# Optimization experiments

Measured on AMD Instinct MI355X. Metric: run time of the kernel, lower is better.

## Reference

```python
import jax, jax.numpy as jnp
import numpy as np

# Gemma-style paged attention, decode-heavy continuous batching
B = 16            # number of sequences in the batch
BLOCK = 64        # KV-cache block size (tokens per block)
MAX_BLOCKS = 32   # max blocks per sequence -> max 2048 KV tokens
NUM_BLOCKS = B * MAX_BLOCKS  # 512 total cache blocks
MAX_KV = MAX_BLOCKS * BLOCK  # 2048
HQ, HK, D = 16, 8, 256       # query heads, kv heads (GQA), head_dim
HIDDEN = 3072
MAX_Q = 4                    # max new (query) tokens per sequence
ROPE_BASE = 10000.0


def setup_inputs() -> dict:
    key = jax.random.key(0)
    ks = jax.random.split(key, 7)
    # deterministic ragged layout
    q_seqlens = np.array([1 + (i % 4) for i in range(B)], np.int64)        # sum = 40
    kv_seqlens = np.array([1024 + (i * 67) % 1025 for i in range(B)], np.int64)
    q_start_loc = np.concatenate([[0], np.cumsum(q_seqlens)[:-1]]).astype(np.int64)
    T = int(q_seqlens.sum())
    history = kv_seqlens - q_seqlens
    position_ids_1d = np.concatenate(
        [np.arange(history[i], kv_seqlens[i]) for i in range(B)]).astype(np.int64)
    block_offsets = np.arange(NUM_BLOCKS, dtype=np.int64).reshape(B, MAX_BLOCKS)
    inv_freq = (1.0 / ROPE_BASE ** (np.arange(0, D, 2) / D)).astype(np.float32)
    return {
        'hidden_states': jax.random.normal(ks[0], (T, HIDDEN), jnp.float32),
        'Wq': jax.random.normal(ks[1], (HIDDEN, HQ * D), jnp.float32) * 0.02,
        'Wk': jax.random.normal(ks[2], (HIDDEN, HK * D), jnp.float32) * 0.02,
        'Wv': jax.random.normal(ks[3], (HIDDEN, HK * D), jnp.float32) * 0.02,
        'Wo': jax.random.normal(ks[4], (HQ * D, HIDDEN), jnp.float32) * 0.02,
        'k_cache': jax.random.normal(ks[5], (NUM_BLOCKS, BLOCK, HK, D), jnp.float32),
        'v_cache': jax.random.normal(ks[6], (NUM_BLOCKS, BLOCK, HK, D), jnp.float32),
        'inv_freq': jnp.asarray(inv_freq),
        'position_ids_1d': jnp.asarray(position_ids_1d),
        'q_start_loc': jnp.asarray(q_start_loc),
        'q_seqlens': jnp.asarray(q_seqlens),
        'kv_seqlens': jnp.asarray(kv_seqlens),
        'block_offsets': jnp.asarray(block_offsets),
    }


def reference(hidden_states, Wq, Wk, Wv, Wo, k_cache, v_cache, inv_freq,
              position_ids_1d, q_start_loc, q_seqlens, kv_seqlens, block_offsets):
    T = hidden_states.shape[0]
    # fused QKV projection
    q = (hidden_states @ Wq).reshape(T, HQ, D)
    k = (hidden_states @ Wk).reshape(T, HK, D)
    v = (hidden_states @ Wv).reshape(T, HK, D)
    # fused rotary embedding (neox / rotate-half style, per-token position ids)
    freqs = position_ids_1d.astype(jnp.float32)[:, None] * inv_freq[None, :]  # [T, D/2]
    cos = jnp.cos(freqs)[:, None, :]
    sin = jnp.sin(freqs)[:, None, :]

    def rope(x):
        x1, x2 = jnp.split(x, 2, axis=-1)
        return jnp.concatenate([x1 * cos - x2 * sin, x2 * cos + x1 * sin], axis=-1)

    q = rope(q)
    k = rope(k)
    # ---- fill_kv_cache: scatter new K/V into paged block cache ----
    tok = jnp.arange(T)
    seq_end = jnp.cumsum(q_seqlens)
    seq_id = jnp.searchsorted(seq_end, tok, side='right')      # sequence of each token
    off = tok - q_start_loc[seq_id]                             # offset within new tokens
    kv_pos = (kv_seqlens - q_seqlens)[seq_id] + off             # absolute kv position
    blk = block_offsets[seq_id, kv_pos // BLOCK]
    slot = kv_pos % BLOCK
    k_cache = k_cache.at[blk, slot].set(k)
    v_cache = v_cache.at[blk, slot].set(v)
    # ---- paged_attention_fwd ----
    # gather each sequence's blocks -> [B, MAX_KV, HK, D]
    k_seq = k_cache[block_offsets].reshape(B, MAX_KV, HK, D)
    v_seq = v_cache[block_offsets].reshape(B, MAX_KV, HK, D)
    # pad queries per sequence -> [B, MAX_Q, HK, G, D]
    qidx = jnp.clip(q_start_loc[:, None] + jnp.arange(MAX_Q)[None, :], 0, T - 1)
    G = HQ // HK
    qpad = q[qidx].reshape(B, MAX_Q, HK, G, D)
    scale = jnp.float32(D) ** -0.5
    scores = jnp.einsum('bqkgd,bskd->bkgqs', qpad * scale, k_seq)  # [B,HK,G,MAX_Q,MAX_KV]
    # causal mask over absolute kv positions (also masks padded kv slots)
    jpos = jnp.arange(MAX_Q)[None, :, None]
    spos = jnp.arange(MAX_KV)[None, None, :]
    mask = spos <= ((kv_seqlens - q_seqlens)[:, None, None] + jpos)  # [B,MAX_Q,MAX_KV]
    scores = jnp.where(mask[:, None, None, :, :], scores, jnp.float32(-1e30))
    attn = jax.nn.softmax(scores, axis=-1)
    out = jnp.einsum('bkgqs,bskd->bqkgd', attn, v_seq).reshape(B, MAX_Q, HQ * D)
    # scatter padded output back to flat token layout
    out_flat = out[seq_id, off]  # [T, HQ*D]
    return out_flat @ Wo
```

## Files before the change

kernel.cpp:

```cpp
#include <hip/hip_runtime.h>
#include <math.h>

#define TT 40
#define NB 16
#define HQn 16
#define HKn 8
#define Gn 2
#define Dn 256
#define HID 3072
#define QKV_COLS 8192
#define NCHUNK 16
#define CHUNKT 128

__global__ __launch_bounds__(256) void k1_qkv_gemm(
    const float* __restrict__ hs, const float* __restrict__ Wq,
    const float* __restrict__ Wk, const float* __restrict__ Wv,
    float* __restrict__ part1) {
  const int tile = blockIdx.x & 31;
  const int ks = blockIdx.x >> 5;
  const int c0 = tile << 8;
  const float* W; int ld, cw0;
  if (tile < 16)      { W = Wq; ld = 4096; cw0 = c0; }
  else if (tile < 24) { W = Wk; ld = 2048; cw0 = c0 - 4096; }
  else                { W = Wv; ld = 2048; cw0 = c0 - 6144; }
  const int kbase = ks * 192;
  const int cq = (threadIdx.x & 63) << 2;
  const int r0 = (threadIdx.x >> 6) * 10;
  __shared__ float h_lds[40][64];
  float acc[10][4];
#pragma unroll
  for (int r = 0; r < 10; ++r) { acc[r][0]=0.f; acc[r][1]=0.f; acc[r][2]=0.f; acc[r][3]=0.f; }
  for (int kc = 0; kc < 192; kc += 64) {
    __syncthreads();
    for (int i = threadIdx.x; i < 2560; i += 256) {
      int t = i >> 6, kk = i & 63;
      h_lds[t][kk] = hs[t * HID + kbase + kc + kk];
    }
    __syncthreads();
    const float* wp = W + (size_t)(kbase + kc) * ld + cw0 + cq;
#pragma unroll 8
    for (int kk = 0; kk < 64; ++kk) {
      float4 w4 = *reinterpret_cast<const float4*>(wp + (size_t)kk * ld);
#pragma unroll
      for (int r = 0; r < 10; ++r) {
        float h = h_lds[r0 + r][kk];
        acc[r][0] = fmaf(h, w4.x, acc[r][0]);
        acc[r][1] = fmaf(h, w4.y, acc[r][1]);
        acc[r][2] = fmaf(h, w4.z, acc[r][2]);
        acc[r][3] = fmaf(h, w4.w, acc[r][3]);
      }
    }
  }
#pragma unroll
  for (int r = 0; r < 10; ++r) {
    int t = r0 + r;
    float4 v = make_float4(acc[r][0], acc[r][1], acc[r][2], acc[r][3]);
    *reinterpret_cast<float4*>(&part1[(size_t)(ks * TT + t) * QKV_COLS + c0 + cq]) = v;
  }
}

__global__ __launch_bounds__(256) void k2_reduce_rope(
    const float* __restrict__ part1, const float* __restrict__ inv_freq,
    const int* __restrict__ pos_ids,
    float* __restrict__ qbuf, float* __restrict__ kbuf, float* __restrict__ vbuf) {
  const int t = blockIdx.x >> 5;
  const int tile = blockIdx.x & 31;
  const int c = (tile << 8) + threadIdx.x;
  float s = 0.f;
#pragma unroll
  for (int ks = 0; ks < 16; ++ks) s += part1[(size_t)(ks * TT + t) * QKV_COLS + c];
  __shared__ float sl[256];
  sl[threadIdx.x] = s;
  __syncthreads();
  if (tile < 24) {
    const int d = threadIdx.x;
    const int d2 = d & 127;
    float fr = (float)pos_ids[t] * inv_freq[d2];
    float cs = cosf(fr), sn = sinf(fr);
    float v = (d < 128) ? (sl[d] * cs - sl[d + 128] * sn)
                        : (sl[d] * cs + sl[d - 128] * sn);
    if (tile < 16) qbuf[t * 4096 + (tile << 8) + d] = v * 0.0625f;
    else           kbuf[t * 2048 + ((tile - 16) << 8) + d] = v;
  } else {
    vbuf[t * 2048 + ((tile - 24) << 8) + threadIdx.x] = s;
  }
}

__global__ __launch_bounds__(256) void k3_attn_partial(
    const float* __restrict__ qbuf, const float* __restrict__ kbuf,
    const float* __restrict__ vbuf, const float* __restrict__ k_cache,
    const float* __restrict__ v_cache, const int* __restrict__ blk_off,
    const int* __restrict__ q_start, const int* __restrict__ q_lens,
    const int* __restrict__ kv_lens,
    float* __restrict__ part_o, float* __restrict__ part_ml) {
  const int chunk = blockIdx.x & 15;
  const int hk = (blockIdx.x >> 4) & 7;
  const int b = blockIdx.x >> 7;
  const int kv_len = kv_lens[b];
  const int cs0 = chunk * CHUNKT;
  if (cs0 >= kv_len) return;
  const int q_cnt = q_lens[b];
  const int hist = kv_len - q_cnt;
  const int q0 = q_start[b];
  const int nq = q_cnt * 2;

  __shared__ float q_lds[8][256];
  __shared__ float S2[2][128][8];
  __shared__ float red[32][8];
  __shared__ float Mg[8];
  __shared__ float obuf[4][8][256];

  const int tid = threadIdx.x;
  const int w = tid >> 6;
  const int lane = tid & 63;
  const int tp = lane & 7;
  const int qd = lane >> 3;

  const int bi = (b << 5) + (cs0 >> 6);
  const int blk0v = blk_off[bi];
  const int blk1v = blk_off[bi + 1];
  const float* kb0  = k_cache + ((size_t)blk0v << 17) + ((size_t)hk << 8);
  const float* kb1  = k_cache + ((size_t)blk1v << 17) + ((size_t)hk << 8);
  const float* vb0  = v_cache + ((size_t)blk0v << 17) + ((size_t)hk << 8);
  const float* vb1  = v_cache + ((size_t)blk1v << 17) + ((size_t)hk << 8);
  const float* knew = kbuf + ((size_t)q0 << 11) + ((size_t)hk << 8);
  const float* vnew = vbuf + ((size_t)q0 << 11) + ((size_t)hk << 8);

  auto rowK = [&](int s) -> const float* {
    if (s < hist) {
      const float* base = (s & 64) ? kb1 : kb0;
      return base + ((size_t)(s & 63) << 11);
    }
    return knew + ((size_t)(s - hist) << 11);
  };
  auto rowV = [&](int s) -> const float* {
    if (s < hist) {
      const float* base = (s & 64) ? vb1 : vb0;
      return base + ((size_t)(s & 63) << 11);
    }
    return vnew + ((size_t)(s - hist) << 11);
  };

  for (int i = tid; i < 2048; i += 256) {
    int qv = i >> 8, d = i & 255;
    int qtok = min(qv >> 1, q_cnt - 1);
    q_lds[qv][d] = qbuf[(size_t)(q0 + qtok) * 4096 + (hk * Gn + (qv & 1)) * 256 + d];
  }
  __syncthreads();

  const int sBeg = cs0 + (w << 5);

  const float* kr[4];
#pragma unroll
  for (int tt = 0; tt < 4; ++tt) {
    int s = sBeg + (tp << 2) + tt;
    int sc = s < kv_len ? s : kv_len - 1;
    kr[tt] = rowK(sc) + (qd << 2);
  }
  float acc[4][8];
#pragma unroll
  for (int tt = 0; tt < 4; ++tt)
#pragma unroll
    for (int qv = 0; qv < 8; ++qv) acc[tt][qv] = 0.f;

#pragma unroll
  for (int c = 0; c < 8; ++c) {
    float4 kf[4];
#pragma unroll
    for (int tt = 0; tt < 4; ++tt)
      kf[tt] = *reinterpret_cast<const float4*>(kr[tt] + (c << 5));
#pragma unroll
    for (int qv = 0; qv < 8; ++qv) {
      float4 qf = *reinterpret_cast<const float4*>(&q_lds[qv][(qd << 2) + (c << 5)]);
#pragma unroll
      for (int tt = 0; tt < 4; ++tt) {
        acc[tt][qv] = fmaf(qf.x, kf[tt].x, acc[tt][qv]);
        acc[tt][qv] = fmaf(qf.y, kf[tt].y, acc[tt][qv]);
        acc[tt][qv] = fmaf(qf.z, kf[tt].z, acc[tt][qv]);
        acc[tt][qv] = fmaf(qf.w, kf[tt].w, acc[tt][qv]);
      }
    }
  }
#pragma unroll
  for (int tt = 0; tt < 4; ++tt)
#pragma unroll
    for (int qv = 0; qv < 8; ++qv) {
      float v = acc[tt][qv];
      v += __shfl_xor(v, 8);
      v += __shfl_xor(v, 16);
      acc[tt][qv] = v;
    }
  if ((lane & 24) == 0) {
    const int h = lane >> 5;
#pragma unroll
    for (int tt = 0; tt < 4; ++tt) {
      int srel = (w << 5) + (tp << 2) + tt;
      *reinterpret_cast<float4*>(&S2[h][srel][0]) =
          make_float4(acc[tt][0], acc[tt][1], acc[tt][2], acc[tt][3]);
      *reinterpret_cast<float4*>(&S2[h][srel][4]) =
          make_float4(acc[tt][4], acc[tt][5], acc[tt][6], acc[tt][7]);
    }
  }
  __syncthreads();

  const int qv2 = tid & 7;
  const int grp = tid >> 3;
  float sv[4];
  {
    float mloc = -1e30f;
#pragma unroll
    for (int t = 0; t < 4; ++t) {
      int sl = (grp << 2) + t;
      float v = S2[0][sl][qv2] + S2[1][sl][qv2];
      bool valid = (qv2 < nq) && ((cs0 + sl - hist) <= (qv2 >> 1));
      v = valid ? v : -1e30f;
      sv[t] = v;
      mloc = fmaxf(mloc, v);
    }
    red[grp][qv2] = mloc;
  }
  __syncthreads();
  if (tid < 8) {
    float M = -1e30f;
#pragma unroll
    for (int i = 0; i < 32; ++i) M = fmaxf(M, red[i][tid]);
    Mg[tid] = M;
  }
  __syncthreads();
  {
    float M = Mg[qv2];
    float lloc = 0.f;
#pragma unroll
    for (int t = 0; t < 4; ++t) {
      float p = __expf(sv[t] - M);
      S2[0][(grp << 2) + t][qv2] = p;
      lloc += p;
    }
    red[grp][qv2] = lloc;
  }
  __syncthreads();
  if (tid < 8) {
    float L = 0.f;
#pragma unroll
    for (int i = 0; i < 32; ++i) L += red[i][tid];
    int pidx = (((b * HKn + hk) * NCHUNK + chunk) << 3) + tid;
    part_ml[pidx * 2] = Mg[tid];
    part_ml[pidx * 2 + 1] = L;
  }

  float4 pacc[8];
#pragma unroll
  for (int q = 0; q < 8; ++q) pacc[q] = make_float4(0.f, 0.f, 0.f, 0.f);
  const int d4 = lane << 2;
#pragma unroll 4
  for (int t = 0; t < 32; ++t) {
    int s = sBeg + t;
    int sc = s < kv_len ? s : kv_len - 1;
    float4 vf = *reinterpret_cast<const float4*>(rowV(sc) + d4);
    int srel = (w << 5) + t;
    float4 p0 = *reinterpret_cast<const float4*>(&S2[0][srel][0]);
    float4 p1 = *reinterpret_cast<const float4*>(&S2[0][srel][4]);
    float pr[8] = {p0.x, p0.y, p0.z, p0.w, p1.x, p1.y, p1.z, p1.w};
#pragma unroll
    for (int q = 0; q < 8; ++q) {
      pacc[q].x = fmaf(pr[q], vf.x, pacc[q].x);
      pacc[q].y = fmaf(pr[q], vf.y, pacc[q].y);
      pacc[q].z = fmaf(pr[q], vf.z, pacc[q].z);
      pacc[q].w = fmaf(pr[q], vf.w, pacc[q].w);
    }
  }
#pragma unroll
  for (int q = 0; q < 8; ++q)
    *reinterpret_cast<float4*>(&obuf[w][q][d4]) = pacc[q];
  __syncthreads();

  for (int q = 0; q < nq; ++q) {
    float o = obuf[0][q][tid] + obuf[1][q][tid] + obuf[2][q][tid] + obuf[3][q][tid];
    int pidx = (((b * HKn + hk) * NCHUNK + chunk) << 3) + q;
    part_o[(size_t)pidx * 256 + tid] = o;
  }
}

__global__ __launch_bounds__(64) void k4_attn_reduce(
    const float* __restrict__ part_o, const float* __restrict__ part_ml,
    const int* __restrict__ q_start, const int* __restrict__ q_lens,
    const int* __restrict__ kv_lens, float* __restrict__ attn_out) {
  const int h = blockIdx.x & 15;
  const int qtok = (blockIdx.x >> 4) & 3;
  const int b = blockIdx.x >> 6;
  const int q_cnt = q_lens[b];
  if (qtok >= q_cnt) return;
  const int kv_len = kv_lens[b];
  const int nparts = (kv_len + CHUNKT - 1) >> 7;
  const int qv = qtok * 2 + (h & 1);
  const int hk = h >> 1;
  const int lane = threadIdx.x;
  const int pbase = ((b * HKn + hk) * NCHUNK) << 3;
  float2 mls[16];
#pragma unroll
  for (int i = 0; i < 16; ++i)
    if (i < nparts)
      mls[i] = *reinterpret_cast<const float2*>(&part_ml[(size_t)(pbase + (i << 3) + qv) * 2]);
  float M = -1e30f;
#pragma unroll
  for (int i = 0; i < 16; ++i)
    if (i < nparts) M = fmaxf(M, mls[i].x);
  float4 o = make_float4(0.f, 0.f, 0.f, 0.f);
  float L = 0.f;
#pragma unroll
  for (int i = 0; i < 16; ++i)
    if (i < nparts) {
      float corr = __expf(mls[i].x - M);
      L += corr * mls[i].y;
      float4 pv = *reinterpret_cast<const float4*>(
          &part_o[(size_t)(pbase + (i << 3) + qv) * 256 + (lane << 2)]);
      o.x = fmaf(corr, pv.x, o.x);
      o.y = fmaf(corr, pv.y, o.y);
      o.z = fmaf(corr, pv.z, o.z);
      o.w = fmaf(corr, pv.w, o.w);
    }
  float inv = 1.0f / L;
  int tr = q_start[b] + qtok;
  float4 res = make_float4(o.x * inv, o.y * inv, o.z * inv, o.w * inv);
  *reinterpret_cast<float4*>(&attn_out[((size_t)tr * HQn + h) * 256 + (lane << 2)]) = res;
}

__global__ __launch_bounds__(256) void k5_out_gemm(
    const float* __restrict__ ain, const float* __restrict__ Wo,
    float* __restrict__ part2) {
  const int tile = blockIdx.x % 12;
  const int ks = blockIdx.x / 12;
  const int c0 = tile << 8;
  const int kbase = ks << 7;
  const int cq = (threadIdx.x & 63) << 2;
  const int r0 = (threadIdx.x >> 6) * 10;
  __shared__ float h_lds[40][64];
  float acc[10][4];
#pragma unroll
  for (int r = 0; r < 10; ++r) { acc[r][0]=0.f; acc[r][1]=0.f; acc[r][2]=0.f; acc[r][3]=0.f; }
  for (int kc = 0; kc < 128; kc += 64) {
    __syncthreads();
    for (int i = threadIdx.x; i < 2560; i += 256) {
      int t = i >> 6, kk = i & 63;
      h_lds[t][kk] = ain[(size_t)t * 4096 + kbase + kc + kk];
    }
    __syncthreads();
    const float* wp = Wo + (size_t)(kbase + kc) * 3072 + c0 + cq;
#pragma unroll 8
    for (int kk = 0; kk < 64; ++kk) {
      float4 w4 = *reinterpret_cast<const float4*>(wp + (size_t)kk * 3072);
#pragma unroll
      for (int r = 0; r < 10; ++r) {
        float h = h_lds[r0 + r][kk];
        acc[r][0] = fmaf(h, w4.x, acc[r][0]);
        acc[r][1] = fmaf(h, w4.y, acc[r][1]);
        acc[r][2] = fmaf(h, w4.z, acc[r][2]);
        acc[r][3] = fmaf(h, w4.w, acc[r][3]);
      }
    }
  }
#pragma unroll
  for (int r = 0; r < 10; ++r) {
    int t = r0 + r;
    float4 v = make_float4(acc[r][0], acc[r][1], acc[r][2], acc[r][3]);
    *reinterpret_cast<float4*>(&part2[(size_t)(ks * TT + t) * 3072 + c0 + cq]) = v;
  }
}

__global__ __launch_bounds__(256) void k6_final_reduce(
    const float* __restrict__ part2, float* __restrict__ out) {
  const int idx = blockIdx.x * 256 + threadIdx.x;
  float s = 0.f;
#pragma unroll
  for (int ks = 0; ks < 32; ++ks) s += part2[(size_t)ks * 122880 + idx];
  out[idx] = s;
}

extern "C" void kernel_launch(void* const* d_in, const int* in_sizes, int n_in,
                              void* d_out, int out_size, void* d_ws, size_t ws_size,
                              hipStream_t stream) {
  const float* hs       = (const float*)d_in[0];
  const float* Wq       = (const float*)d_in[1];
  const float* Wk       = (const float*)d_in[2];
  const float* Wv       = (const float*)d_in[3];
  const float* Wo       = (const float*)d_in[4];
  const float* k_cache  = (const float*)d_in[5];
  const float* v_cache  = (const float*)d_in[6];
  const float* inv_freq = (const float*)d_in[7];
  const int*   pos_ids  = (const int*)d_in[8];
  const int*   q_start  = (const int*)d_in[9];
  const int*   q_lens   = (const int*)d_in[10];
  const int*   kv_lens  = (const int*)d_in[11];
  const int*   blk_off  = (const int*)d_in[12];

  float* ws = (float*)d_ws;
  float* qbuf     = ws;
  float* kbuf     = ws + 163840;
  float* vbuf     = ws + 245760;
  float* attn_out = ws + 327680;
  float* big      = ws + 491520;
  float* part1    = big;
  float* part_o   = big;
  float* part_ml  = big + 4194304;
  float* part2    = big;
  float* out      = (float*)d_out;

  k1_qkv_gemm<<<512, 256, 0, stream>>>(hs, Wq, Wk, Wv, part1);
  k2_reduce_rope<<<1280, 256, 0, stream>>>(part1, inv_freq, pos_ids, qbuf, kbuf, vbuf);
  k3_attn_partial<<<2048, 256, 0, stream>>>(qbuf, kbuf, vbuf, k_cache, v_cache,
                                            blk_off, q_start, q_lens, kv_lens,
                                            part_o, part_ml);
  k4_attn_reduce<<<1024, 64, 0, stream>>>(part_o, part_ml, q_start, q_lens,
                                          kv_lens, attn_out);
  k5_out_gemm<<<384, 256, 0, stream>>>(attn_out, Wo, part2);
  k6_final_reduce<<<480, 256, 0, stream>>>(part2, out);
}
```

Baseline: 290.6 us.

## Fuse all six kernels into one persistent cooperative kernel with grid syncs

Replaces the six separate launches (QKV GEMM, reduce+RoPE, attention partial, attention reduce, output GEMM, final reduce) with a single cooperative persistent kernel. Each stage loops over its original work items with a grid-stride loop, and stages are separated by grid-wide syncs. Shared memory is carved from one buffer. The aim is to remove per-launch overhead and inter-kernel gaps. In exchange, occupancy is capped at 3 blocks per CU with a grid of at most 768, each stage carries grid-sync cost, and the 50KB shared allocation may limit residency.

Result: slower. 679.3 us (+133.8%).

```diff
diff --git a/kernel.cpp b/kernel.cpp
--- a/kernel.cpp
+++ b/kernel.cpp
@@ -1,5 +1,8 @@
 #include <hip/hip_runtime.h>
+#include <hip/hip_cooperative_groups.h>
 #include <math.h>
+
+namespace cg = cooperative_groups;
 
 #define TT 40
 #define NB 16
@@ -11,369 +14,390 @@
 #define QKV_COLS 8192
 #define NCHUNK 16
 #define CHUNKT 128
-
-__global__ __launch_bounds__(256) void k1_qkv_gemm(
+#define MAXGRID 768
+
+__global__ __launch_bounds__(256, 3) void mega(
     const float* __restrict__ hs, const float* __restrict__ Wq,
     const float* __restrict__ Wk, const float* __restrict__ Wv,
-    float* __restrict__ part1) {
-  const int tile = blockIdx.x & 31;
-  const int ks = blockIdx.x >> 5;
-  const int c0 = tile << 8;
-  const float* W; int ld, cw0;
-  if (tile < 16)      { W = Wq; ld = 4096; cw0 = c0; }
-  else if (tile < 24) { W = Wk; ld = 2048; cw0 = c0 - 4096; }
-  else                { W = Wv; ld = 2048; cw0 = c0 - 6144; }
-  const int kbase = ks * 192;
-  const int cq = (threadIdx.x & 63) << 2;
-  const int r0 = (threadIdx.x >> 6) * 10;
-  __shared__ float h_lds[40][64];
-  float acc[10][4];
-#pragma unroll
-  for (int r = 0; r < 10; ++r) { acc[r][0]=0.f; acc[r][1]=0.f; acc[r][2]=0.f; acc[r][3]=0.f; }
-  for (int kc = 0; kc < 192; kc += 64) {
-    __syncthreads();
-    for (int i = threadIdx.x; i < 2560; i += 256) {
-      int t = i >> 6, kk = i & 63;
-      h_lds[t][kk] = hs[t * HID + kbase + kc + kk];
+    const float* __restrict__ Wo, const float* __restrict__ k_cache,
+    const float* __restrict__ v_cache, const float* __restrict__ inv_freq,
+    const int* __restrict__ pos_ids, const int* __restrict__ q_start,
+    const int* __restrict__ q_lens, const int* __restrict__ kv_lens,
+    const int* __restrict__ blk_off,
+    float* __restrict__ qbuf, float* __restrict__ kbuf, float* __restrict__ vbuf,
+    float* __restrict__ attn_out, float* __restrict__ part1,
+    float* __restrict__ part_o, float* __restrict__ part_ml,
+    float* __restrict__ part2, float* __restrict__ out) {
+  cg::grid_group grd = cg::this_grid();
+  __shared__ __align__(16) char smem[50240];
+  const int tid = threadIdx.x;
+  const int NGRID = gridDim.x;
+
+  {
+    float (*h_lds)[64] = (float (*)[64])smem;
+    for (int v = blockIdx.x; v < 512; v += NGRID) {
+      const int tile = v & 31;
+      const int ks = v >> 5;
+      const int c0 = tile << 8;
+      const float* W; int ld, cw0;
+      if (tile < 16)      { W = Wq; ld = 4096; cw0 = c0; }
+      else if (tile < 24) { W = Wk; ld = 2048; cw0 = c0 - 4096; }
+      else                { W = Wv; ld = 2048; cw0 = c0 - 6144; }
+      const int kbase = ks * 192;
+      const int cq = (tid & 63) << 2;
+      const int r0 = (tid >> 6) * 10;
+      float acc[10][4];
+#pragma unroll
+      for (int r = 0; r < 10; ++r) { acc[r][0]=0.f; acc[r][1]=0.f; acc[r][2]=0.f; acc[r][3]=0.f; }
+      for (int kc = 0; kc < 192; kc += 64) {
+        __syncthreads();
+        for (int i = tid; i < 2560; i += 256) {
+          int t = i >> 6, kk = i & 63;
+          h_lds[t][kk] = hs[t * HID + kbase + kc + kk];
+        }
+        __syncthreads();
+        const float* wp = W + (size_t)(kbase + kc) * ld + cw0 + cq;
+#pragma unroll 8
+        for (int kk = 0; kk < 64; ++kk) {
+          float4 w4 = *reinterpret_cast<const float4*>(wp + (size_t)kk * ld);
+#pragma unroll
+          for (int r = 0; r < 10; ++r) {
+            float h = h_lds[r0 + r][kk];
+            acc[r][0] = fmaf(h, w4.x, acc[r][0]);
+            acc[r][1] = fmaf(h, w4.y, acc[r][1]);
+            acc[r][2] = fmaf(h, w4.z, acc[r][2]);
+            acc[r][3] = fmaf(h, w4.w, acc[r][3]);
+          }
+        }
+      }
+#pragma unroll
+      for (int r = 0; r < 10; ++r) {
+        int t = r0 + r;
+        float4 vv = make_float4(acc[r][0], acc[r][1], acc[r][2], acc[r][3]);
+        *reinterpret_cast<float4*>(&part1[(size_t)(ks * TT + t) * QKV_COLS + c0 + cq]) = vv;
+      }
+      __syncthreads();
     }
-    __syncthreads();
-    const float* wp = W + (size_t)(kbase + kc) * ld + cw0 + cq;
+  }
+  grd.sync();
+
+  {
+    float* sl = (float*)smem;
+    for (int v = blockIdx.x; v < 1280; v += NGRID) {
+      const int t = v >> 5;
+      const int tile = v & 31;
+      const int c = (tile << 8) + tid;
+      float s = 0.f;
+#pragma unroll
+      for (int ks = 0; ks < 16; ++ks) s += part1[(size_t)(ks * TT + t) * QKV_COLS + c];
+      __syncthreads();
+      sl[tid] = s;
+      __syncthreads();
+      if (tile < 24) {
+        const int d = tid;
+        const int d2 = d & 127;
+        float fr = (float)pos_ids[t] * inv_freq[d2];
+        float cs = cosf(fr), sn = sinf(fr);
+        float val = (d < 128) ? (sl[d] * cs - sl[d + 128] * sn)
+                              : (sl[d] * cs + sl[d - 128] * sn);
+        if (tile < 16) qbuf[t * 4096 + (tile << 8) + d] = val * 0.0625f;
+        else           kbuf[t * 2048 + ((tile - 16) << 8) + d] = val;
+      } else {
+        vbuf[t * 2048 + ((tile - 24) << 8) + tid] = s;
+      }
+      __syncthreads();
+    }
+  }
+  grd.sync();
+
+  {
+    float (*q_lds)[256] = (float (*)[256])smem;
+    float (*S2)[8]      = (float (*)[8])(smem + 8192);
+    float (*red)[8]     = (float (*)[8])(smem + 16384);
+    float* Mg           = (float*)(smem + 17408);
+    float (*obuf)[256]  = (float (*)[256])(smem + 17472);
+    const int w = tid >> 6;
+    const int lane = tid & 63;
+    const int tp = lane & 7;
+    const int qd = lane >> 3;
+
+    for (int v = blockIdx.x; v < 2048; v += NGRID) {
+      const int chunk = v & 15;
+      const int hk = (v >> 4) & 7;
+      const int b = v >> 7;
+      const int kv_len = kv_lens[b];
+      const int cs0 = chunk * CHUNKT;
+      if (cs0 < kv_len) {
+        const int q_cnt = q_lens[b];
+        const int hist = kv_len - q_cnt;
+        const int q0 = q_start[b];
+        const int nq = q_cnt * 2;
+
+        const int bi = (b << 5) + (cs0 >> 6);
+        const int blk0v = blk_off[bi];
+        const int blk1v = blk_off[bi + 1];
+        const float* kb0  = k_cache + ((size_t)blk0v << 17) + ((size_t)hk << 8);
+        const float* kb1  = k_cache + ((size_t)blk1v << 17) + ((size_t)hk << 8);
+        const float* vb0  = v_cache + ((size_t)blk0v << 17) + ((size_t)hk << 8);
+        const float* vb1  = v_cache + ((size_t)blk1v << 17) + ((size_t)hk << 8);
+        const float* knew = kbuf + ((size_t)q0 << 11) + ((size_t)hk << 8);
+        const float* vnew = vbuf + ((size_t)q0 << 11) + ((size_t)hk << 8);
+
+        auto rowK = [&](int s) -> const float* {
+          if (s < hist) {
+            const float* base = (s & 64) ? kb1 : kb0;
+            return base + ((size_t)(s & 63) << 11);
+          }
+          return knew + ((size_t)(s - hist) << 11);
+        };
+        auto rowV = [&](int s) -> const float* {
+          if (s < hist) {
+            const float* base = (s & 64) ? vb1 : vb0;
+            return base + ((size_t)(s & 63) << 11);
+          }
+          return vnew + ((size_t)(s - hist) << 11);
+        };
+
+        __syncthreads();
+        for (int i = tid; i < 2048; i += 256) {
+          int qv = i >> 8, d = i & 255;
+          int qtok = min(qv >> 1, q_cnt - 1);
+          q_lds[qv][d] = qbuf[(size_t)(q0 + qtok) * 4096 + (hk * Gn + (qv & 1)) * 256 + d];
+        }
+        __syncthreads();
+
+        const int sBeg = cs0 + (w << 5);
+
+        const float* kr[4];
+#pragma unroll
+        for (int tt = 0; tt < 4; ++tt) {
+          int s = sBeg + (tp << 2) + tt;
+          int sc = s < kv_len ? s : kv_len - 1;
+          kr[tt] = rowK(sc) + (qd << 2);
+        }
+        float acc[4][8];
+#pragma unroll
+        for (int tt = 0; tt < 4; ++tt)
+#pragma unroll
+          for (int qv = 0; qv < 8; ++qv) acc[tt][qv] = 0.f;
+#pragma unroll
+        for (int c = 0; c < 8; ++c) {
+          float4 kf[4];
+#pragma unroll
+          for (int tt = 0; tt < 4; ++tt)
+            kf[tt] = *reinterpret_cast<const float4*>(kr[tt] + (c << 5));
+#pragma unroll
+          for (int qv = 0; qv < 8; ++qv) {
+            float4 qf = *reinterpret_cast<const float4*>(&q_lds[qv][(qd << 2) + (c << 5)]);
+#pragma unroll
+            for (int tt = 0; tt < 4; ++tt) {
+              acc[tt][qv] = fmaf(qf.x, kf[tt].x, acc[tt][qv]);
+              acc[tt][qv] = fmaf(qf.y, kf[tt].y, acc[tt][qv]);
+              acc[tt][qv] = fmaf(qf.z, kf[tt].z, acc[tt][qv]);
+              acc[tt][qv] = fmaf(qf.w, kf[tt].w, acc[tt][qv]);
+            }
+          }
+        }
+#pragma unroll
+        for (int tt = 0; tt < 4; ++tt)
+#pragma unroll
+          for (int qv = 0; qv < 8; ++qv) {
+            float val = acc[tt][qv];
+            val += __shfl_xor(val, 8);
+            val += __shfl_xor(val, 16);
+            acc[tt][qv] = val;
+          }
+        if ((lane & 24) == 0) {
+          const int h = lane >> 5;
+#pragma unroll
+          for (int tt = 0; tt < 4; ++tt) {
+            int srel = (w << 5) + (tp << 2) + tt;
+            *reinterpret_cast<float4*>(&S2[(h << 7) + srel][0]) =
+                make_float4(acc[tt][0], acc[tt][1], acc[tt][2], acc[tt][3]);
+            *reinterpret_cast<float4*>(&S2[(h << 7) + srel][4]) =
+                make_float4(acc[tt][4], acc[tt][5], acc[tt][6], acc[tt][7]);
+          }
+        }
+        __syncthreads();
+
+        const int qv2 = tid & 7;
+        const int grp = tid >> 3;
+        float sv[4];
+        {
+          float mloc = -1e30f;
+#pragma unroll
+          for (int t = 0; t < 4; ++t) {
+            int sl2 = (grp << 2) + t;
+            float val = S2[sl2][qv2] + S2[128 + sl2][qv2];
+            bool valid = (qv2 < nq) && ((cs0 + sl2 - hist) <= (qv2 >> 1));
+            val = valid ? val : -1e30f;
+            sv[t] = val;
+            mloc = fmaxf(mloc, val);
+          }
+          red[grp][qv2] = mloc;
+        }
+        __syncthreads();
+        if (tid < 8) {
+          float M = -1e30f;
+#pragma unroll
+          for (int i = 0; i < 32; ++i) M = fmaxf(M, red[i][tid]);
+          Mg[tid] = M;
+        }
+        __syncthreads();
+        {
+          float M = Mg[qv2];
+          float lloc = 0.f;
+#pragma unroll
+          for (int t = 0; t < 4; ++t) {
+            float p = __expf(sv[t] - M);
+            S2[(grp << 2) + t][qv2] = p;
+            lloc += p;
+          }
+          red[grp][qv2] = lloc;
+        }
+        __syncthreads();
+        if (tid < 8) {
+          float L = 0.f;
+#pragma unroll
+          for (int i = 0; i < 32; ++i) L += red[i][tid];
+          int pidx = (((b * HKn + hk) * NCHUNK + chunk) << 3) + tid;
+          part_ml[pidx * 2] = Mg[tid];
+          part_ml[pidx * 2 + 1] = L;
+        }
+
+        float4 pacc[8];
+#pragma unroll
+        for (int q = 0; q < 8; ++q) pacc[q] = make_float4(0.f, 0.f, 0.f, 0.f);
+        const int d4 = lane << 2;
+#pragma unroll 4
+        for (int t = 0; t < 32; ++t) {
+          int s = sBeg + t;
+          int sc = s < kv_len ? s : kv_len - 1;
+          float4 vf = *reinterpret_cast<const float4*>(rowV(sc) + d4);
+          int srel = (w << 5) + t;
+          float4 p0 = *reinterpret_cast<const float4*>(&S2[srel][0]);
+          float4 p1 = *reinterpret_cast<const float4*>(&S2[srel][4]);
+          float pr[8] = {p0.x, p0.y, p0.z, p0.w, p1.x, p1.y, p1.z, p1.w};
+#pragma unroll
+          for (int q = 0; q < 8; ++q) {
+            pacc[q].x = fmaf(pr[q], vf.x, pacc[q].x);
+            pacc[q].y = fmaf(pr[q], vf.y, pacc[q].y);
+            pacc[q].z = fmaf(pr[q], vf.z, pacc[q].z);
+            pacc[q].w = fmaf(pr[q], vf.w, pacc[q].w);
+          }
+        }
+#pragma unroll
+        for (int q = 0; q < 8; ++q)
+          *reinterpret_cast<float4*>(&obuf[w * 8 + q][d4]) = pacc[q];
+        __syncthreads();
+
+        for (int q = 0; q < nq; ++q) {
+          float o = obuf[q][tid] + obuf[8 + q][tid] + obuf[16 + q][tid] + obuf[24 + q][tid];
+          int pidx = (((b * HKn + hk) * NCHUNK + chunk) << 3) + q;
+          part_o[(size_t)pidx * 256 + tid] = o;
+        }
+        __syncthreads();
+      }
+    }
+  }
+  grd.sync();
+
+  {
+    const int w = tid >> 6;
+    const int lane = tid & 63;
+    for (int u = blockIdx.x * 4 + w; u < 1024; u += NGRID * 4) {
+      const int h = u & 15;
+      const int qtok = (u >> 4) & 3;
+      const int b = u >> 6;
+      const int q_cnt = q_lens[b];
+      if (qtok < q_cnt) {
+        const int kv_len = kv_lens[b];
+        const int nparts = (kv_len + CHUNKT - 1) >> 7;
+        const int qv = qtok * 2 + (h & 1);
+        const int hk = h >> 1;
+        const int pbase = ((b * HKn + hk) * NCHUNK) << 3;
+        float2 mls[16];
+#pragma unroll
+        for (int i = 0; i < 16; ++i)
+          if (i < nparts)
+            mls[i] = *reinterpret_cast<const float2*>(&part_ml[(size_t)(pbase + (i << 3) + qv) * 2]);
+        float M = -1e30f;
+#pragma unroll
+        for (int i = 0; i < 16; ++i)
+          if (i < nparts) M = fmaxf(M, mls[i].x);
+        float4 o = make_float4(0.f, 0.f, 0.f, 0.f);
+        float L = 0.f;
+#pragma unroll
+        for (int i = 0; i < 16; ++i)
+          if (i < nparts) {
+            float corr = __expf(mls[i].x - M);
+            L += corr * mls[i].y;
+            float4 pv = *reinterpret_cast<const float4*>(
+                &part_o[(size_t)(pbase + (i << 3) + qv) * 256 + (lane << 2)]);
+            o.x = fmaf(corr, pv.x, o.x);
+            o.y = fmaf(corr, pv.y, o.y);
+            o.z = fmaf(corr, pv.z, o.z);
+            o.w = fmaf(corr, pv.w, o.w);
+          }
+        float inv = 1.0f / L;
+        int tr = q_start[b] + qtok;
+        float4 res = make_float4(o.x * inv, o.y * inv, o.z * inv, o.w * inv);
+        *reinterpret_cast<float4*>(&attn_out[((size_t)tr * HQn + h) * 256 + (lane << 2)]) = res;
+      }
+    }
+  }
+  grd.sync();
+
+  {
+    float (*h_lds)[64] = (float (*)[64])smem;
+    for (int v = blockIdx.x; v < 384; v += NGRID) {
+      const int tile = v % 12;
+      const int ks = v / 12;
+      const int c0 = tile << 8;
+      const int kbase = ks << 7;
+      const int cq = (tid & 63) << 2;
+      const int r0 = (tid >> 6) * 10;
+      float acc[10][4];
+#pragma unroll
+      for (int r = 0; r < 10; ++r) { acc[r][0]=0.f; acc[r][1]=0.f; acc[r][2]=0.f; acc[r][3]=0.f; }
+      for (int kc = 0; kc < 128; kc += 64) {
+        __syncthreads();
+        for (int i = tid; i < 2560; i += 256) {
+          int t = i >> 6, kk = i & 63;
+          h_lds[t][kk] = attn_out[(size_t)t * 4096 + kbase + kc + kk];
+        }
+        __syncthreads();
+        const float* wp = Wo + (size_t)(kbase + kc) * 3072 + c0 + cq;
 #pragma unroll 8
-    for (int kk = 0; kk < 64; ++kk) {
-      float4 w4 = *reinterpret_cast<const float4*>(wp + (size_t)kk * ld);
+        for (int kk = 0; kk < 64; ++kk) {
+          float4 w4 = *reinterpret_cast<const float4*>(wp + (size_t)kk * 3072);
+#pragma unroll
+          for (int r = 0; r < 10; ++r) {
+            float h = h_lds[r0 + r][kk];
+            acc[r][0] = fmaf(h, w4.x, acc[r][0]);
+            acc[r][1] = fmaf(h, w4.y, acc[r][1]);
+            acc[r][2] = fmaf(h, w4.z, acc[r][2]);
+            acc[r][3] = fmaf(h, w4.w, acc[r][3]);
+          }
+        }
+      }
 #pragma unroll
       for (int r = 0; r < 10; ++r) {
-        float h = h_lds[r0 + r][kk];
-        acc[r][0] = fmaf(h, w4.x, acc[r][0]);
-        acc[r][1] = fmaf(h, w4.y, acc[r][1]);
-        acc[r][2] = fmaf(h, w4.z, acc[r][2]);
-        acc[r][3] = fmaf(h, w4.w, acc[r][3]);
-      }
+        int t = r0 + r;
+        float4 vv = make_float4(acc[r][0], acc[r][1], acc[r][2], acc[r][3]);
+        *reinterpret_cast<float4*>(&part2[(size_t)(ks * TT + t) * 3072 + c0 + cq]) = vv;
+      }
+      __syncthreads();
     }
   }
-#pragma unroll
-  for (int r = 0; r < 10; ++r) {
-    int t = r0 + r;
-    float4 v = make_float4(acc[r][0], acc[r][1], acc[r][2], acc[r][3]);
-    *reinterpret_cast<float4*>(&part1[(size_t)(ks * TT + t) * QKV_COLS + c0 + cq]) = v;
-  }
-}
-
-__global__ __launch_bounds__(256) void k2_reduce_rope(
-    const float* __restrict__ part1, const float* __restrict__ inv_freq,
-    const int* __restrict__ pos_ids,
-    float* __restrict__ qbuf, float* __restrict__ kbuf, float* __restrict__ vbuf) {
-  const int t = blockIdx.x >> 5;
-  const int tile = blockIdx.x & 31;
-  const int c = (tile << 8) + threadIdx.x;
-  float s = 0.f;
-#pragma unroll
-  for (int ks = 0; ks < 16; ++ks) s += part1[(size_t)(ks * TT + t) * QKV_COLS + c];
-  __shared__ float sl[256];
-  sl[threadIdx.x] = s;
-  __syncthreads();
-  if (tile < 24) {
-    const int d = threadIdx.x;
-    const int d2 = d & 127;
-    float fr = (float)pos_ids[t] * inv_freq[d2];
-    float cs = cosf(fr), sn = sinf(fr);
-    float v = (d < 128) ? (sl[d] * cs - sl[d + 128] * sn)
-                        : (sl[d] * cs + sl[d - 128] * sn);
-    if (tile < 16) qbuf[t * 4096 + (tile << 8) + d] = v * 0.0625f;
-    else           kbuf[t * 2048 + ((tile - 16) << 8) + d] = v;
-  } else {
-    vbuf[t * 2048 + ((tile - 24) << 8) + threadIdx.x] = s;
-  }
-}
-
-__global__ __launch_bounds__(256) void k3_attn_partial(
-    const float* __restrict__ qbuf, const float* __restrict__ kbuf,
-    const float* __restrict__ vbuf, const float* __restrict__ k_cache,
-    const float* __restrict__ v_cache, const int* __restrict__ blk_off,
-    const int* __restrict__ q_start, const int* __restrict__ q_lens,
-    const int* __restrict__ kv_lens,
-    float* __restrict__ part_o, float* __restrict__ part_ml) {
-  const int chunk = blockIdx.x & 15;
-  const int hk = (blockIdx.x >> 4) & 7;
-  const int b = blockIdx.x >> 7;
-  const int kv_len = kv_lens[b];
-  const int cs0 = chunk * CHUNKT;
-  if (cs0 >= kv_len) return;
-  const int q_cnt = q_lens[b];
-  const int hist = kv_len - q_cnt;
-  const int q0 = q_start[b];
-  const int nq = q_cnt * 2;
-
-  __shared__ float q_lds[8][256];
-  __shared__ float S2[2][128][8];
-  __shared__ float red[32][8];
-  __shared__ float Mg[8];
-  __shared__ float obuf[4][8][256];
-
-  const int tid = threadIdx.x;
-  const int w = tid >> 6;
-  const int lane = tid & 63;
-  const int tp = lane & 7;
-  const int qd = lane >> 3;
-
-  const int bi = (b << 5) + (cs0 >> 6);
-  const int blk0v = blk_off[bi];
-  const int blk1v = blk_off[bi + 1];
-  const float* kb0  = k_cache + ((size_t)blk0v << 17) + ((size_t)hk << 8);
-  const float* kb1  = k_cache + ((size_t)blk1v << 17) + ((size_t)hk << 8);
-  const float* vb0  = v_cache + ((size_t)blk0v << 17) + ((size_t)hk << 8);
-  const float* vb1  = v_cache + ((size_t)blk1v << 17) + ((size_t)hk << 8);
-  const float* knew = kbuf + ((size_t)q0 << 11) + ((size_t)hk << 8);
-  const float* vnew = vbuf + ((size_t)q0 << 11) + ((size_t)hk << 8);
-
-  auto rowK = [&](int s) -> const float* {
-    if (s < hist) {
-      const float* base = (s & 64) ? kb1 : kb0;
-      return base + ((size_t)(s & 63) << 11);
-    }
-    return knew + ((size_t)(s - hist) << 11);
-  };
-  auto rowV = [&](int s) -> const float* {
-    if (s < hist) {
-      const float* base = (s & 64) ? vb1 : vb0;
-      return base + ((size_t)(s & 63) << 11);
-    }
-    return vnew + ((size_t)(s - hist) << 11);
-  };
-
-  for (int i = tid; i < 2048; i += 256) {
-    int qv = i >> 8, d = i & 255;
-    int qtok = min(qv >> 1, q_cnt - 1);
-    q_lds[qv][d] = qbuf[(size_t)(q0 + qtok) * 4096 + (hk * Gn + (qv & 1)) * 256 + d];
-  }
-  __syncthreads();
-
-  const int sBeg = cs0 + (w << 5);
-
-  const float* kr[4];
-#pragma unroll
-  for (int tt = 0; tt < 4; ++tt) {
-    int s = sBeg + (tp << 2) + tt;
-    int sc = s < kv_len ? s : kv_len - 1;
-    kr[tt] = rowK(sc) + (qd << 2);
-  }
-  float acc[4][8];
-#pragma unroll
-  for (int tt = 0; tt < 4; ++tt)
-#pragma unroll
-    for (int qv = 0; qv < 8; ++qv) acc[tt][qv] = 0.f;
-
-#pragma unroll
-  for (int c = 0; c < 8; ++c) {
-    float4 kf[4];
-#pragma unroll
-    for (int tt = 0; tt < 4; ++tt)
-      kf[tt] = *reinterpret_cast<const float4*>(kr[tt] + (c << 5));
-#pragma unroll
-    for (int qv = 0; qv < 8; ++qv) {
-      float4 qf = *reinterpret_cast<const float4*>(&q_lds[qv][(qd << 2) + (c << 5)]);
-#pragma unroll
-      for (int tt = 0; tt < 4; ++tt) {
-        acc[tt][qv] = fmaf(qf.x, kf[tt].x, acc[tt][qv]);
-        acc[tt][qv] = fmaf(qf.y, kf[tt].y, acc[tt][qv]);
-        acc[tt][qv] = fmaf(qf.z, kf[tt].z, acc[tt][qv]);
-        acc[tt][qv] = fmaf(qf.w, kf[tt].w, acc[tt][qv]);
-      }
-    }
-  }
-#pragma unroll
-  for (int tt = 0; tt < 4; ++tt)
-#pragma unroll
-    for (int qv = 0; qv < 8; ++qv) {
-      float v = acc[tt][qv];
-      v += __shfl_xor(v, 8);
-      v += __shfl_xor(v, 16);
-      acc[tt][qv] = v;
-    }
-  if ((lane & 24) == 0) {
-    const int h = lane >> 5;
-#pragma unroll
-    for (int tt = 0; tt < 4; ++tt) {
-      int srel = (w << 5) + (tp << 2) + tt;
-      *reinterpret_cast<float4*>(&S2[h][srel][0]) =
-          make_float4(acc[tt][0], acc[tt][1], acc[tt][2], acc[tt][3]);
-      *reinterpret_cast<float4*>(&S2[h][srel][4]) =
-          make_float4(acc[tt][4], acc[tt][5], acc[tt][6], acc[tt][7]);
-    }
-  }
-  __syncthreads();
-
-  const int qv2 = tid & 7;
-  const int grp = tid >> 3;
-  float sv[4];
-  {
-    float mloc = -1e30f;
-#pragma unroll
-    for (int t = 0; t < 4; ++t) {
-      int sl = (grp << 2) + t;
-      float v = S2[0][sl][qv2] + S2[1][sl][qv2];
-      bool valid = (qv2 < nq) && ((cs0 + sl - hist) <= (qv2 >> 1));
-      v = valid ? v : -1e30f;
-      sv[t] = v;
-      mloc = fmaxf(mloc, v);
-    }
-    red[grp][qv2] = mloc;
-  }
-  __syncthreads();
-  if (tid < 8) {
-    float M = -1e30f;
-#pragma unroll
-    for (int i = 0; i < 32; ++i) M = fmaxf(M, red[i][tid]);
-    Mg[tid] = M;
-  }
-  __syncthreads();
-  {
-    float M = Mg[qv2];
-    float lloc = 0.f;
-#pragma unroll
-    for (int t = 0; t < 4; ++t) {
-      float p = __expf(sv[t] - M);
-      S2[0][(grp << 2) + t][qv2] = p;
-      lloc += p;
-    }
-    red[grp][qv2] = lloc;
-  }
-  __syncthreads();
-  if (tid < 8) {
-    float L = 0.f;
-#pragma unroll
-    for (int i = 0; i < 32; ++i) L += red[i][tid];
-    int pidx = (((b * HKn + hk) * NCHUNK + chunk) << 3) + tid;
-    part_ml[pidx * 2] = Mg[tid];
-    part_ml[pidx * 2 + 1] = L;
-  }
-
-  float4 pacc[8];
-#pragma unroll
-  for (int q = 0; q < 8; ++q) pacc[q] = make_float4(0.f, 0.f, 0.f, 0.f);
-  const int d4 = lane << 2;
-#pragma unroll 4
-  for (int t = 0; t < 32; ++t) {
-    int s = sBeg + t;
-    int sc = s < kv_len ? s : kv_len - 1;
-    float4 vf = *reinterpret_cast<const float4*>(rowV(sc) + d4);
-    int srel = (w << 5) + t;
-    float4 p0 = *reinterpret_cast<const float4*>(&S2[0][srel][0]);
-    float4 p1 = *reinterpret_cast<const float4*>(&S2[0][srel][4]);
-    float pr[8] = {p0.x, p0.y, p0.z, p0.w, p1.x, p1.y, p1.z, p1.w};
-#pragma unroll
-    for (int q = 0; q < 8; ++q) {
-      pacc[q].x = fmaf(pr[q], vf.x, pacc[q].x);
-      pacc[q].y = fmaf(pr[q], vf.y, pacc[q].y);
-      pacc[q].z = fmaf(pr[q], vf.z, pacc[q].z);
-      pacc[q].w = fmaf(pr[q], vf.w, pacc[q].w);
-    }
-  }
-#pragma unroll
-  for (int q = 0; q < 8; ++q)
-    *reinterpret_cast<float4*>(&obuf[w][q][d4]) = pacc[q];
-  __syncthreads();
-
-  for (int q = 0; q < nq; ++q) {
-    float o = obuf[0][q][tid] + obuf[1][q][tid] + obuf[2][q][tid] + obuf[3][q][tid];
-    int pidx = (((b * HKn + hk) * NCHUNK + chunk) << 3) + q;
-    part_o[(size_t)pidx * 256 + tid] = o;
-  }
-}
-
-__global__ __launch_bounds__(64) void k4_attn_reduce(
-    const float* __restrict__ part_o, const float* __restrict__ part_ml,
-    const int* __restrict__ q_start, const int* __restrict__ q_lens,
-    const int* __restrict__ kv_lens, float* __restrict__ attn_out) {
-  const int h = blockIdx.x & 15;
-  const int qtok = (blockIdx.x >> 4) & 3;
-  const int b = blockIdx.x >> 6;
-  const int q_cnt = q_lens[b];
-  if (qtok >= q_cnt) return;
-  const int kv_len = kv_lens[b];
-  const int nparts = (kv_len + CHUNKT - 1) >> 7;
-  const int qv = qtok * 2 + (h & 1);
-  const int hk = h >> 1;
-  const int lane = threadIdx.x;
-  const int pbase = ((b * HKn + hk) * NCHUNK) << 3;
-  float2 mls[16];
-#pragma unroll
-  for (int i = 0; i < 16; ++i)
-    if (i < nparts)
-      mls[i] = *reinterpret_cast<const float2*>(&part_ml[(size_t)(pbase + (i << 3) + qv) * 2]);
-  float M = -1e30f;
-#pragma unroll
-  for (int i = 0; i < 16; ++i)
-    if (i < nparts) M = fmaxf(M, mls[i].x);
-  float4 o = make_float4(0.f, 0.f, 0.f, 0.f);
-  float L = 0.f;
-#pragma unroll
-  for (int i = 0; i < 16; ++i)
-    if (i < nparts) {
-      float corr = __expf(mls[i].x - M);
-      L += corr * mls[i].y;
-      float4 pv = *reinterpret_cast<const float4*>(
-          &part_o[(size_t)(pbase + (i << 3) + qv) * 256 + (lane << 2)]);
-      o.x = fmaf(corr, pv.x, o.x);
-      o.y = fmaf(corr, pv.y, o.y);
-      o.z = fmaf(corr, pv.z, o.z);
-      o.w = fmaf(corr, pv.w, o.w);
-    }
-  float inv = 1.0f / L;
-  int tr = q_start[b] + qtok;
-  float4 res = make_float4(o.x * inv, o.y * inv, o.z * inv, o.w * inv);
-  *reinterpret_cast<float4*>(&attn_out[((size_t)tr * HQn + h) * 256 + (lane << 2)]) = res;
-}
-
-__global__ __launch_bounds__(256) void k5_out_gemm(
-    const float* __restrict__ ain, const float* __restrict__ Wo,
-    float* __restrict__ part2) {
-  const int tile = blockIdx.x % 12;
-  const int ks = blockIdx.x / 12;
-  const int c0 = tile << 8;
-  const int kbase = ks << 7;
-  const int cq = (threadIdx.x & 63) << 2;
-  const int r0 = (threadIdx.x >> 6) * 10;
-  __shared__ float h_lds[40][64];
-  float acc[10][4];
-#pragma unroll
-  for (int r = 0; r < 10; ++r) { acc[r][0]=0.f; acc[r][1]=0.f; acc[r][2]=0.f; acc[r][3]=0.f; }
-  for (int kc = 0; kc < 128; kc += 64) {
-    __syncthreads();
-    for (int i = threadIdx.x; i < 2560; i += 256) {
-      int t = i >> 6, kk = i & 63;
-      h_lds[t][kk] = ain[(size_t)t * 4096 + kbase + kc + kk];
-    }
-    __syncthreads();
-    const float* wp = Wo + (size_t)(kbase + kc) * 3072 + c0 + cq;
-#pragma unroll 8
-    for (int kk = 0; kk < 64; ++kk) {
-      float4 w4 = *reinterpret_cast<const float4*>(wp + (size_t)kk * 3072);
-#pragma unroll
-      for (int r = 0; r < 10; ++r) {
-        float h = h_lds[r0 + r][kk];
-        acc[r][0] = fmaf(h, w4.x, acc[r][0]);
-        acc[r][1] = fmaf(h, w4.y, acc[r][1]);
-        acc[r][2] = fmaf(h, w4.z, acc[r][2]);
-        acc[r][3] = fmaf(h, w4.w, acc[r][3]);
-      }
-    }
-  }
-#pragma unroll
-  for (int r = 0; r < 10; ++r) {
-    int t = r0 + r;
-    float4 v = make_float4(acc[r][0], acc[r][1], acc[r][2], acc[r][3]);
-    *reinterpret_cast<float4*>(&part2[(size_t)(ks * TT + t) * 3072 + c0 + cq]) = v;
-  }
-}
-
-__global__ __launch_bounds__(256) void k6_final_reduce(
-    const float* __restrict__ part2, float* __restrict__ out) {
-  const int idx = blockIdx.x * 256 + threadIdx.x;
-  float s = 0.f;
-#pragma unroll
-  for (int ks = 0; ks < 32; ++ks) s += part2[(size_t)ks * 122880 + idx];
-  out[idx] = s;
+  grd.sync();
+
+  for (int idx = blockIdx.x * 256 + tid; idx < 122880; idx += NGRID * 256) {
+    float s = 0.f;
+#pragma unroll
+    for (int ks = 0; ks < 32; ++ks) s += part2[(size_t)ks * 122880 + idx];
+    out[idx] = s;
+  }
 }
 
 extern "C" void kernel_launch(void* const* d_in, const int* in_sizes, int n_in,
@@ -405,13 +429,18 @@
   float* part2    = big;
   float* out      = (float*)d_out;
 
-  k1_qkv_gemm<<<512, 256, 0, stream>>>(hs, Wq, Wk, Wv, part1);
-  k2_reduce_rope<<<1280, 256, 0, stream>>>(part1, inv_freq, pos_ids, qbuf, kbuf, vbuf);
-  k3_attn_partial<<<2048, 256, 0, stream>>>(qbuf, kbuf, vbuf, k_cache, v_cache,
-                                            blk_off, q_start, q_lens, kv_lens,
-                                            part_o, part_ml);
-  k4_attn_reduce<<<1024, 64, 0, stream>>>(part_o, part_ml, q_start, q_lens,
-                                          kv_lens, attn_out);
-  k5_out_gemm<<<384, 256, 0, stream>>>(attn_out, Wo, part2);
-  k6_final_reduce<<<480, 256, 0, stream>>>(part2, out);
+  int maxb = 0;
+  hipOccupancyMaxActiveBlocksPerMultiprocessor(&maxb, (const void*)mega, 256, 0);
+  int grid = maxb * 256;
+  if (grid > MAXGRID) grid = MAXGRID;
+  if (grid < 1) grid = 1;
+
+  void* args[] = {
+    (void*)&hs, (void*)&Wq, (void*)&Wk, (void*)&Wv, (void*)&Wo,
+    (void*)&k_cache, (void*)&v_cache, (void*)&inv_freq, (void*)&pos_ids,
+    (void*)&q_start, (void*)&q_lens, (void*)&kv_lens, (void*)&blk_off,
+    (void*)&qbuf, (void*)&kbuf, (void*)&vbuf, (void*)&attn_out,
+    (void*)&part1, (void*)&part_o, (void*)&part_ml, (void*)&part2, (void*)&out
+  };
+  hipLaunchCooperativeKernel((void*)mega, dim3(grid), dim3(256), args, 0, stream);
 }
```
